# Performance work log

Measured on AMD Instinct MI355X. Metric: run time of the kernel, lower is better.

Reference implementation:

```python
import jax, jax.numpy as jnp
import numpy as np

# Geometry constants (from config)
H, D_BOT, P, K, D = 4096, 1024, 8, 64, 64
SCALE = 1.0


def setup_inputs() -> dict:
    key = jax.random.key(0)
    ks = jax.random.split(key, 20)
    B, T = 4, 2048

    def lin(k, din, dout, s=0.02):
        kw, kb = jax.random.split(k)
        return (jax.random.normal(kw, (din, dout), jnp.float32) * s,
                jax.random.normal(kb, (dout,), jnp.float32) * s)

    x = jax.random.normal(ks[0], (B, T, H), jnp.float32)
    Wi, bi = lin(ks[1], H, D_BOT)
    Wb, bb = lin(ks[2], D_BOT, P * D)          # base_coord_proj
    Wf, bf = lin(ks[3], D_BOT, P * K)          # fiber_section_proj
    Wl, bl = lin(ks[4], D_BOT, P * (D + K))    # lambda_term_proj
    Ww, bw = lin(ks[5], D_BOT, P)              # mixture_proj_w
    Wm, bm = lin(ks[6], D_BOT, P * D)          # mixture_proj_m
    Ws, bs = lin(ks[7], D_BOT, P * D)          # mixture_proj_s
    Wu, bu = lin(ks[8], D_BOT, P * K)          # mixture_proj_u
    Wo, bo = lin(ks[9], D + K, H)              # output_proj
    return dict(x=x, Wi=Wi, bi=bi, Wb=Wb, bb=bb, Wf=Wf, bf=bf, Wl=Wl, bl=bl,
                Ww=Ww, bw=bw, Wm=Wm, bm=bm, Ws=Ws, bs=bs, Wu=Wu, bu=bu,
                Wo=Wo, bo=bo)


def reference(x, Wi, bi, Wb, bb, Wf, bf, Wl, bl, Ww, bw, Wm, bm, Ws, bs, Wu, bu, Wo, bo):
    B, T, _ = x.shape
    # Shared bottleneck
    h_bot = jnp.einsum('bth,hd->btd', x, Wi) + bi                      # (B,T,D_bot)

    # Fan-out of small parallel projections (fused-QKV-like opportunity)
    base_coords = (jnp.einsum('btd,de->bte', h_bot, Wb) + bb).reshape(B, T, P, D)
    base_coords = jnp.clip(base_coords, -10.0, 10.0)
    fiber_sections = (jnp.einsum('btd,de->bte', h_bot, Wf) + bf).reshape(B, T, P, K)
    lambda_terms = (jnp.einsum('btd,de->bte', h_bot, Wl) + bl).reshape(B, T, P, D + K)
    w_logits = jnp.einsum('btd,dp->btp', h_bot, Ww) + bw               # (B,T,P)
    m = (jnp.einsum('btd,de->bte', h_bot, Wm) + bm).reshape(B, T, P, D)
    log_s = jnp.clip((jnp.einsum('btd,de->bte', h_bot, Ws) + bs).reshape(B, T, P, D), -5.0, 5.0)
    u = (jnp.einsum('btd,de->bte', h_bot, Wu) + bu).reshape(B, T, P, K)

    # Lambda operations / info-geometric update treated as identity (undefined in source)
    updated_sections = fiber_sections

    # Parallel transport correction along the T axis: curr - 0.1*(curr - prev)
    prev = base_coords[:, :-1]
    curr = base_coords[:, 1:]
    transported = jnp.concatenate(
        [base_coords[:, :1], curr - 0.1 * (curr - prev)], axis=1)       # (B,T,P,D)
    updated_coords = transported

    # Mixture aggregation
    weights = jax.nn.softmax(w_logits, axis=-1)                         # (B,T,P)
    agg_coords = jnp.einsum('btp,btpd->btd', weights, updated_coords)   # (B,T,D)
    agg_sections = jnp.einsum('btp,btpk->btk', weights, updated_sections)  # (B,T,K)

    combined = jnp.concatenate([agg_coords, agg_sections], axis=-1)     # (B,T,D+K)
    output = jnp.einsum('bte,eh->bth', combined, Wo) + bo               # (B,T,H)
    return x + SCALE * output
```

## Files before the change

### kernel.cpp

```cpp
#include <hip/hip_runtime.h>
#include <hip/hip_bf16.h>
#include <stdint.h>

typedef __hip_bfloat16 bf16;
typedef __attribute__((ext_vector_type(8))) short short8;
typedef __attribute__((ext_vector_type(4))) short short4_t;
typedef __attribute__((ext_vector_type(4))) float float4_t;

__device__ __forceinline__ short f2b_bits(float f) {
  union { float f; unsigned u; } v; v.f = f;
  unsigned r = (v.u + 0x7FFF + ((v.u >> 16) & 1)) >> 16;
  return (short)r;
}
__device__ __forceinline__ bf16 f2b(float f) {
  short s = f2b_bits(f);
  bf16 h; __builtin_memcpy(&h, &s, 2);
  return h;
}
__device__ __forceinline__ bf16 ld_bf16(const void* p, size_t idx, int f32) {
  if (f32) return f2b(((const float*)p)[idx]);
  return ((const bf16*)p)[idx];
}

__device__ __forceinline__ void gload_lds16(const void* g, void* l) {
  __builtin_amdgcn_global_load_lds(
      (const __attribute__((address_space(1))) void*)g,
      (__attribute__((address_space(3))) void*)l, 16, 0, 0);
}

__global__ void detect_dtype(const void* probe, int* flag) {
  int lane = threadIdx.x;
  const unsigned short* u = (const unsigned short*)probe;
  const float* fp = (const float*)probe;
  int cb = 0, cf = 0;
  for (int j = lane; j < 256; j += 64) {
    unsigned short he = u[2 * j];
    int e = (he >> 7) & 0xFF;
    cb += (e >= 0x60 && e <= 0x7E);
    float af = fabsf(fp[j]);
    cf += (af > 1e-9f && af < 1.0f);
  }
#pragma unroll
  for (int off = 32; off > 0; off >>= 1) {
    cb += __shfl_down(cb, off);
    cf += __shfl_down(cf, off);
  }
  if (lane == 0) *flag = (cf > cb) ? 1 : 0;
}

__global__ __launch_bounds__(256) void cvt_x(const void* __restrict__ x,
                                             bf16* __restrict__ xb,
                                             const int* __restrict__ flagp,
                                             size_t n) {
  const int f32 = *flagp;
  size_t i = ((size_t)blockIdx.x * 256 + threadIdx.x) * 8;
  size_t stride = (size_t)gridDim.x * 256 * 8;
  for (; i < n; i += stride) {
    if (f32) {
      const float* xp = (const float*)x + i;
      float4_t f0 = *(const float4_t*)xp;
      float4_t f1 = *(const float4_t*)(xp + 4);
      short8 v;
      v[0] = f2b_bits(f0[0]); v[1] = f2b_bits(f0[1]);
      v[2] = f2b_bits(f0[2]); v[3] = f2b_bits(f0[3]);
      v[4] = f2b_bits(f1[0]); v[5] = f2b_bits(f1[1]);
      v[6] = f2b_bits(f1[2]); v[7] = f2b_bits(f1[3]);
      *(short8*)(xb + i) = v;
    } else {
      *(short8*)(xb + i) = *(const short8*)((const bf16*)x + i);
    }
  }
}

__global__ __launch_bounds__(256) void transpose_all(
    const void* __restrict__ Wi, const void* __restrict__ Wb,
    const void* __restrict__ Wf, const void* __restrict__ Wo,
    bf16* __restrict__ WiT, bf16* __restrict__ WbfT2, bf16* __restrict__ WoT,
    const int* __restrict__ flagp)
{
  const int f32 = *flagp;
  int b = blockIdx.x;
  const void* src; bf16* dst; int K, N, tb;
  if (b < 1024)      { src = Wi; dst = WiT;              K = 4096; N = 1024; tb = b; }
  else if (b < 1152) { src = Wb; dst = WbfT2;            K = 1024; N = 512;  tb = b - 1024; }
  else if (b < 1280) { src = Wf; dst = WbfT2 + 512*1024; K = 1024; N = 512;  tb = b - 1152; }
  else               { src = Wo; dst = WoT;              K = 128;  N = 4096; tb = b - 1280; }
  int nbk = K >> 6;
  int kb = (tb % nbk) * 64, nb = (tb / nbk) * 64;
  __shared__ bf16 tile[64][65];
  int tx = threadIdx.x & 63;
  int ty = threadIdx.x >> 6;
#pragma unroll
  for (int i = 0; i < 64; i += 4)
    tile[ty + i][tx] = ld_bf16(src, (size_t)(kb + ty + i) * N + nb + tx, f32);
  __syncthreads();
#pragma unroll
  for (int i = 0; i < 64; i += 4)
    dst[(size_t)(nb + ty + i) * K + kb + tx] = tile[tx][ty + i];
}

__global__ __launch_bounds__(256) void cvt_small(
    const void* __restrict__ Ww, const void* __restrict__ bw,
    const void* __restrict__ bi, const void* __restrict__ bb,
    const void* __restrict__ bf_, const void* __restrict__ bo,
    bf16* __restrict__ WbfT2, bf16* __restrict__ bbf2,
    bf16* __restrict__ biC, bf16* __restrict__ boC,
    const int* __restrict__ flagp)
{
  const int f32 = *flagp;
  int i = blockIdx.x * 256 + threadIdx.x;
  if (i < 131072) {
    int r = i >> 10, k = i & 1023;
    bf16 v = (r < 8) ? ld_bf16(Ww, (size_t)k * 8 + r, f32) : f2b(0.f);
    WbfT2[(size_t)(1024 + r) * 1024 + k] = v;
  }
  if (i < 128) bbf2[1024 + i] = (i < 8) ? ld_bf16(bw, i, f32) : f2b(0.f);
  if (i < 1024) biC[i] = ld_bf16(bi, i, f32);
  if (i < 512)  bbf2[i] = ld_bf16(bb, i, f32);
  if (i < 512)  bbf2[512 + i] = ld_bf16(bf_, i, f32);
  if (i < 4096) boC[i] = ld_bf16(bo, i, f32);
}

__device__ __forceinline__ void epilogue_64x128(
    char* smem, float4_t (&acc)[2][4], const bf16* bias, const void* resid,
    void* C, int rf32, int cf32, int m0, int n0, int N, int clip_cols,
    int tid, int lane, int wm, int wn, int lm)
{
  float* EP = (float*)smem;
  const int ep_c = (tid & 15) * 4;
#pragma unroll
  for (int h = 0; h < 2; h++) {
    if ((wn >> 6) == h) {
#pragma unroll
      for (int mi = 0; mi < 2; mi++)
#pragma unroll
        for (int ni = 0; ni < 4; ni++) {
          int cl = (wn - h * 64) + ni * 16 + lm;
#pragma unroll
          for (int r = 0; r < 4; r++) {
            int rw = wm + mi * 16 + (lane >> 4) * 4 + r;
            EP[rw * 68 + cl] = acc[mi][ni][r];
          }
        }
    }
    __syncthreads();
#pragma unroll
    for (int i = 0; i < 4; i++) {
      int rw  = (tid >> 4) + 16 * i;
      int gr  = m0 + rw;
      int col = n0 + h * 64 + ep_c;
      size_t idx = (size_t)gr * N + col;
      float4_t v = *(const float4_t*)(EP + rw * 68 + ep_c);
      float o[4];
#pragma unroll
      for (int j = 0; j < 4; j++) {
        float t = v[j] + __bfloat162float(bias[col + j]);
        if (col + j < clip_cols) t = fminf(fmaxf(t, -10.f), 10.f);
        o[j] = t;
      }
      if (resid) {
        if (rf32) {
          float4_t rv = *(const float4_t*)((const float*)resid + idx);
#pragma unroll
          for (int j = 0; j < 4; j++) o[j] += rv[j];
        } else {
          short4_t rv = *(const short4_t*)((const bf16*)resid + idx);
#pragma unroll
          for (int j = 0; j < 4; j++) {
            bf16 hb; short sb = rv[j]; __builtin_memcpy(&hb, &sb, 2);
            o[j] += __bfloat162float(hb);
          }
        }
      }
      if (cf32) {
        *(float4_t*)((float*)C + idx) = (float4_t){o[0], o[1], o[2], o[3]};
      } else {
        short4_t pv;
#pragma unroll
        for (int j = 0; j < 4; j++) pv[j] = f2b_bits(o[j]);
        *(short4_t*)((bf16*)C + idx) = pv;
      }
    }
    __syncthreads();
  }
}

__device__ __forceinline__ void gemm_core_db(
    const bf16* __restrict__ A,
    const bf16* __restrict__ BT,
    const bf16* __restrict__ bias,
    const void* __restrict__ resid,
    void* __restrict__ C,
    const int* __restrict__ rF32, const int* __restrict__ cF32,
    int M, int N, int K, int clip_cols)
{
  constexpr int BM = 64, BN = 128;
  __shared__ alignas(16) char smem[2 * (BM + BN) * 64 * 2];
  bf16* As0 = (bf16*)smem;
  bf16* As1 = (bf16*)(smem + 16384 / 2);
  bf16* Bs0 = (bf16*)(smem + 16384);
  bf16* Bs1 = (bf16*)(smem + 16384 + 16384);
  const int rf32 = rF32 ? *rF32 : 0;
  const int cf32 = cF32 ? *cF32 : 0;
  const int tid  = threadIdx.x;
  const int wave = tid >> 6;
  const int lane = tid & 63;
  const int m0 = blockIdx.x * BM;
  const int n0 = blockIdx.y * BN;
  const int wm = (wave >> 1) * (BM / 2);
  const int wn = (wave & 1) * (BN / 2);
  const int lm = lane & 15;
  const int lk = (lane >> 4) * 8;

  auto stage = [&](bf16* as, bf16* bs, int k0) {
#pragma unroll
    for (int i = 0; i < BN / 32; i++) {
      int V = tid + 256 * i;
      gload_lds16(BT + (size_t)(n0 + (V >> 3)) * K + k0 + (V & 7) * 8,
                  bs + (size_t)V * 8);
    }
#pragma unroll
    for (int i = 0; i < BM / 32; i++) {
      int V = tid + 256 * i;
      gload_lds16(A + (size_t)(m0 + (V >> 3)) * K + k0 + (V & 7) * 8,
                  as + (size_t)V * 8);
    }
  };

  float4_t acc[2][4];
#pragma unroll
  for (int i = 0; i < 2; i++)
#pragma unroll
    for (int j = 0; j < 4; j++) acc[i][j] = (float4_t){0.f, 0.f, 0.f, 0.f};

  const int NT = K >> 6;
  stage(As0, Bs0, 0);

  for (int t = 0; t < NT; t++) {
    bf16* Asc = (t & 1) ? As1 : As0;
    bf16* Bsc = (t & 1) ? Bs1 : Bs0;
    if (t + 1 < NT) {
      stage((t & 1) ? As0 : As1, (t & 1) ? Bs0 : Bs1, (t + 1) << 6);
      asm volatile("s_waitcnt vmcnt(6)" ::: "memory");
    } else {
      asm volatile("s_waitcnt vmcnt(0)" ::: "memory");
    }
    __builtin_amdgcn_sched_barrier(0);
    __builtin_amdgcn_s_barrier();
    __builtin_amdgcn_sched_barrier(0);
#pragma unroll
    for (int kk = 0; kk < 64; kk += 32) {
      short8 af[2], bfr[4];
#pragma unroll
      for (int mi = 0; mi < 2; mi++)
        af[mi] = *(const short8*)(Asc + (wm + mi * 16 + lm) * 64 + kk + lk);
#pragma unroll
      for (int ni = 0; ni < 4; ni++)
        bfr[ni] = *(const short8*)(Bsc + (wn + ni * 16 + lm) * 64 + kk + lk);
#pragma unroll
      for (int mi = 0; mi < 2; mi++)
#pragma unroll
        for (int ni = 0; ni < 4; ni++)
          acc[mi][ni] = __builtin_amdgcn_mfma_f32_16x16x32_bf16(
              af[mi], bfr[ni], acc[mi][ni], 0, 0, 0);
    }
    __builtin_amdgcn_sched_barrier(0);
    __builtin_amdgcn_s_barrier();
  }
  epilogue_64x128(smem, acc, bias, resid, C, rf32, cf32,
                  m0, n0, N, clip_cols, tid, lane, wm, wn, lm);
}

__device__ __forceinline__ void gemm_core_sb(
    const void* __restrict__ A, const bf16* __restrict__ BT,
    const bf16* __restrict__ bias, const void* __restrict__ resid,
    void* __restrict__ C, const int* __restrict__ aF32,
    const int* __restrict__ rF32, const int* __restrict__ cF32,
    int M, int N, int K, int clip_cols)
{
  constexpr int BM = 64, BN = 128;
  __shared__ alignas(16) char smem[(BM + BN) * 64 * 2];
  bf16* As = (bf16*)smem;
  bf16* Bs = (bf16*)smem + BM * 64;
  const int af32 = aF32 ? *aF32 : 0;
  const int rf32 = rF32 ? *rF32 : 0;
  const int cf32 = cF32 ? *cF32 : 0;
  const int tid  = threadIdx.x;
  const int wave = tid >> 6;
  const int lane = tid & 63;
  const int m0 = blockIdx.x * BM;
  const int n0 = blockIdx.y * BN;
  const int wm = (wave >> 1) * (BM / 2);
  const int wn = (wave & 1) * (BN / 2);
  const int lm = lane & 15;
  const int lk = (lane >> 4) * 8;

  float4_t acc[2][4];
#pragma unroll
  for (int i = 0; i < 2; i++)
#pragma unroll
    for (int j = 0; j < 4; j++) acc[i][j] = (float4_t){0.f, 0.f, 0.f, 0.f};

  for (int k0 = 0; k0 < K; k0 += 64) {
#pragma unroll
    for (int i = 0; i < BN / 32; i++) {
      int V = tid + 256 * i;
      gload_lds16(BT + (size_t)(n0 + (V >> 3)) * K + k0 + (V & 7) * 8,
                  Bs + (size_t)V * 8);
    }
#pragma unroll
    for (int i = 0; i < BM / 32; i++) {
      int V = tid + 256 * i;
      int row = V >> 3, kc = (V & 7) * 8;
      if (af32) {
        const float* ap = (const float*)A + (size_t)(m0 + row) * K + k0 + kc;
        float4_t f0 = *(const float4_t*)ap;
        float4_t f1 = *(const float4_t*)(ap + 4);
        short8 v;
        v[0] = f2b_bits(f0[0]); v[1] = f2b_bits(f0[1]);
        v[2] = f2b_bits(f0[2]); v[3] = f2b_bits(f0[3]);
        v[4] = f2b_bits(f1[0]); v[5] = f2b_bits(f1[1]);
        v[6] = f2b_bits(f1[2]); v[7] = f2b_bits(f1[3]);
        *(short8*)(As + (size_t)V * 8) = v;
      } else {
        gload_lds16((const bf16*)A + (size_t)(m0 + row) * K + k0 + kc,
                    As + (size_t)V * 8);
      }
    }
    __syncthreads();
#pragma unroll
    for (int kk = 0; kk < 64; kk += 32) {
      short8 af[2], bfr[4];
#pragma unroll
      for (int mi = 0; mi < 2; mi++)
        af[mi] = *(const short8*)(As + (wm + mi * 16 + lm) * 64 + kk + lk);
#pragma unroll
      for (int ni = 0; ni < 4; ni++)
        bfr[ni] = *(const short8*)(Bs + (wn + ni * 16 + lm) * 64 + kk + lk);
#pragma unroll
      for (int mi = 0; mi < 2; mi++)
#pragma unroll
        for (int ni = 0; ni < 4; ni++)
          acc[mi][ni] = __builtin_amdgcn_mfma_f32_16x16x32_bf16(
              af[mi], bfr[ni], acc[mi][ni], 0, 0, 0);
    }
    __syncthreads();
  }
  epilogue_64x128(smem, acc, bias, resid, C, rf32, cf32,
                  m0, n0, N, clip_cols, tid, lane, wm, wn, lm);
}

__global__ __launch_bounds__(256) void gemm_x(
    const bf16* A, const bf16* BT, const bf16* bias, const void* resid,
    void* C, const int* rF32, const int* cF32, int M, int N, int K, int clip_cols) {
  gemm_core_db(A, BT, bias, resid, C, rF32, cF32, M, N, K, clip_cols);
}
__global__ __launch_bounds__(256) void gemm_x_f(
    const void* A, const bf16* BT, const bf16* bias, const void* resid,
    void* C, const int* aF32, const int* rF32, const int* cF32,
    int M, int N, int K, int clip_cols) {
  gemm_core_sb(A, BT, bias, resid, C, aF32, rF32, cF32, M, N, K, clip_cols);
}
__global__ __launch_bounds__(256) void gemm_h(
    const bf16* A, const bf16* BT, const bf16* bias, const void* resid,
    void* C, const int* rF32, const int* cF32, int M, int N, int K, int clip_cols) {
  gemm_core_db(A, BT, bias, resid, C, rF32, cF32, M, N, K, clip_cols);
}
__global__ __launch_bounds__(256) void gemm_o(
    const bf16* A, const bf16* BT, const bf16* bias, const void* resid,
    void* C, const int* rF32, const int* cF32, int M, int N, int K, int clip_cols) {
  gemm_core_db(A, BT, bias, resid, C, rF32, cF32, M, N, K, clip_cols);
}

__global__ __launch_bounds__(128) void build_combined(
    const bf16* __restrict__ bcfs,
    bf16* __restrict__ comb)
{
  int t = blockIdx.x;
  int tid = threadIdx.x;
  int tl = t & 2047;
  __shared__ float lg[8];
  __shared__ float w[8];
  if (tid < 8) lg[tid] = __bfloat162float(bcfs[(size_t)t * 1152 + 1024 + tid]);
  __syncthreads();
  if (tid < 8) {
    float mx = lg[0];
#pragma unroll
    for (int i = 1; i < 8; i++) mx = fmaxf(mx, lg[i]);
    float den = 0.f;
#pragma unroll
    for (int i = 0; i < 8; i++) den += expf(lg[i] - mx);
    w[tid] = expf(lg[tid] - mx) / den;
  }
  __syncthreads();
  float s = 0.f;
  if (tid < 64) {
    int d = tid;
    const bf16* bc = bcfs + (size_t)t * 1152;
    size_t tp = (tl == 0) ? (size_t)t : (size_t)t - 1;
    const bf16* bp = bcfs + tp * 1152;
#pragma unroll
    for (int p = 0; p < 8; p++) {
      float cur = __bfloat162float(bc[p * 64 + d]);
      float v = (tl == 0) ? cur : (0.9f * cur + 0.1f * __bfloat162float(bp[p * 64 + d]));
      s += w[p] * v;
    }
  } else {
    int d = tid - 64;
    const bf16* fsrow = bcfs + (size_t)t * 1152 + 512;
#pragma unroll
    for (int p = 0; p < 8; p++) s += w[p] * __bfloat162float(fsrow[p * 64 + d]);
  }
  comb[(size_t)t * 128 + tid] = __float2bfloat16(s);
}

extern "C" void kernel_launch(void* const* d_in, const int* in_sizes, int n_in,
                              void* d_out, int out_size, void* d_ws, size_t ws_size,
                              hipStream_t stream) {
  (void)in_sizes; (void)n_in; (void)out_size;
  const void* x   = d_in[0];
  const void* Wi  = d_in[1];
  const void* bi  = d_in[2];
  const void* Wb  = d_in[3];
  const void* bb  = d_in[4];
  const void* Wf  = d_in[5];
  const void* bfv = d_in[6];
  const void* Ww  = d_in[9];
  const void* bw  = d_in[10];
  const void* Wo  = d_in[17];
  const void* bo  = d_in[18];

  char* ws = (char*)d_ws;
  bf16*  h_bot = (bf16*)(ws + 0);
  bf16*  comb  = (bf16*)(ws + 0);
  bf16*  bcfs  = (bf16*)(ws + 16777216);
  bf16*  WiT   = (bf16*)(ws + 35651584);
  bf16*  WbfT2 = (bf16*)(ws + 44040192);
  bf16*  WoT   = (bf16*)(ws + 46399488);
  bf16*  biC   = (bf16*)(ws + 47448064);
  bf16*  bbf2C = (bf16*)(ws + 47450112);
  bf16*  boC   = (bf16*)(ws + 47452416);
  int*   flag  = (int*)(ws + 47460608);
  bf16*  xb    = (bf16*)(ws + 47464448);
  const bool use_xb = ws_size >= (size_t)47464448 + 67108864;

  detect_dtype<<<1, 64, 0, stream>>>(bi, flag);

  if (use_xb)
    cvt_x<<<2048, 256, 0, stream>>>(x, xb, flag, (size_t)8192 * 4096);

  transpose_all<<<1408, 256, 0, stream>>>(Wi, Wb, Wf, Wo, WiT, WbfT2, WoT, flag);
  cvt_small<<<512, 256, 0, stream>>>(Ww, bw, bi, bb, bfv, bo,
                                     WbfT2, bbf2C, biC, boC, flag);

  if (use_xb)
    gemm_x<<<dim3(128, 8), 256, 0, stream>>>(
        xb, WiT, biC, nullptr, h_bot, nullptr, nullptr,
        8192, 1024, 4096, 0);
  else
    gemm_x_f<<<dim3(128, 8), 256, 0, stream>>>(
        x, WiT, biC, nullptr, h_bot, flag, nullptr, nullptr,
        8192, 1024, 4096, 0);
  gemm_h<<<dim3(128, 9), 256, 0, stream>>>(
      h_bot, WbfT2, bbf2C, nullptr, bcfs, nullptr, nullptr,
      8192, 1152, 1024, 512);
  build_combined<<<8192, 128, 0, stream>>>(bcfs, comb);
  gemm_o<<<dim3(128, 32), 256, 0, stream>>>(
      comb, WoT, boC, x, d_out, flag, flag,
      8192, 4096, 128, 0);
}
```

Before: 528.2 us.

## Stage A tile through registers and fuse x conversion into transpose kernel

```diff
diff --git a/kernel.cpp b/kernel.cpp
--- a/kernel.cpp
+++ b/kernel.cpp
@@ -48,38 +48,36 @@
   if (lane == 0) *flag = (cf > cb) ? 1 : 0;
 }
 
-__global__ __launch_bounds__(256) void cvt_x(const void* __restrict__ x,
-                                             bf16* __restrict__ xb,
-                                             const int* __restrict__ flagp,
-                                             size_t n) {
-  const int f32 = *flagp;
-  size_t i = ((size_t)blockIdx.x * 256 + threadIdx.x) * 8;
-  size_t stride = (size_t)gridDim.x * 256 * 8;
-  for (; i < n; i += stride) {
-    if (f32) {
-      const float* xp = (const float*)x + i;
-      float4_t f0 = *(const float4_t*)xp;
-      float4_t f1 = *(const float4_t*)(xp + 4);
-      short8 v;
-      v[0] = f2b_bits(f0[0]); v[1] = f2b_bits(f0[1]);
-      v[2] = f2b_bits(f0[2]); v[3] = f2b_bits(f0[3]);
-      v[4] = f2b_bits(f1[0]); v[5] = f2b_bits(f1[1]);
-      v[6] = f2b_bits(f1[2]); v[7] = f2b_bits(f1[3]);
-      *(short8*)(xb + i) = v;
-    } else {
-      *(short8*)(xb + i) = *(const short8*)((const bf16*)x + i);
-    }
-  }
-}
-
 __global__ __launch_bounds__(256) void transpose_all(
     const void* __restrict__ Wi, const void* __restrict__ Wb,
     const void* __restrict__ Wf, const void* __restrict__ Wo,
     bf16* __restrict__ WiT, bf16* __restrict__ WbfT2, bf16* __restrict__ WoT,
+    const void* __restrict__ x, bf16* __restrict__ xb,
     const int* __restrict__ flagp)
 {
   const int f32 = *flagp;
   int b = blockIdx.x;
+  if (b >= 1408) {
+    size_t base = (size_t)(b - 1408) * 16384;
+#pragma unroll
+    for (int j = 0; j < 8; j++) {
+      size_t i = base + (size_t)j * 2048 + threadIdx.x * 8;
+      if (f32) {
+        const float* xp = (const float*)x + i;
+        float4_t f0 = *(const float4_t*)xp;
+        float4_t f1 = *(const float4_t*)(xp + 4);
+        short8 v;
+        v[0] = f2b_bits(f0[0]); v[1] = f2b_bits(f0[1]);
+        v[2] = f2b_bits(f0[2]); v[3] = f2b_bits(f0[3]);
+        v[4] = f2b_bits(f1[0]); v[5] = f2b_bits(f1[1]);
+        v[6] = f2b_bits(f1[2]); v[7] = f2b_bits(f1[3]);
+        *(short8*)(xb + i) = v;
+      } else {
+        *(short8*)(xb + i) = *(const short8*)((const bf16*)x + i);
+      }
+    }
+    return;
+  }
   const void* src; bf16* dst; int K, N, tb;
   if (b < 1024)      { src = Wi; dst = WiT;              K = 4096; N = 1024; tb = b; }
   else if (b < 1152) { src = Wb; dst = WbfT2;            K = 1024; N = 512;  tb = b - 1024; }
@@ -185,21 +183,17 @@
   }
 }
 
-__device__ __forceinline__ void gemm_core_db(
-    const bf16* __restrict__ A,
-    const bf16* __restrict__ BT,
-    const bf16* __restrict__ bias,
-    const void* __restrict__ resid,
-    void* __restrict__ C,
-    const int* __restrict__ rF32, const int* __restrict__ cF32,
-    int M, int N, int K, int clip_cols)
+__device__ __forceinline__ void gemm_core_db2(
+    const bf16* __restrict__ A, const bf16* __restrict__ BT,
+    const bf16* __restrict__ bias, const void* __restrict__ resid,
+    void* __restrict__ C, const int* __restrict__ rF32,
+    const int* __restrict__ cF32, int M, int N, int K, int clip_cols)
 {
   constexpr int BM = 64, BN = 128;
-  __shared__ alignas(16) char smem[2 * (BM + BN) * 64 * 2];
-  bf16* As0 = (bf16*)smem;
-  bf16* As1 = (bf16*)(smem + 16384 / 2);
-  bf16* Bs0 = (bf16*)(smem + 16384);
-  bf16* Bs1 = (bf16*)(smem + 16384 + 16384);
+  __shared__ alignas(16) char smem[(BM * 64 + 2 * BN * 64) * 2];
+  bf16* As  = (bf16*)smem;
+  bf16* Bs0 = (bf16*)(smem + BM * 64 * 2);
+  bf16* Bs1 = (bf16*)(smem + BM * 64 * 2 + BN * 64 * 2);
   const int rf32 = rF32 ? *rF32 : 0;
   const int cf32 = cF32 ? *cF32 : 0;
   const int tid  = threadIdx.x;
@@ -212,19 +206,28 @@
   const int lm = lane & 15;
   const int lk = (lane >> 4) * 8;
 
-  auto stage = [&](bf16* as, bf16* bs, int k0) {
-#pragma unroll
-    for (int i = 0; i < BN / 32; i++) {
+  short8 areg[2];
+  auto loadA = [&](int k0) {
+#pragma unroll
+    for (int i = 0; i < 2; i++) {
+      int V = tid + 256 * i;
+      areg[i] = *(const short8*)(A + (size_t)(m0 + (V >> 3)) * K + k0 + (V & 7) * 8);
+    }
+  };
+  auto writeA = [&]() {
+#pragma unroll
+    for (int i = 0; i < 2; i++) {
+      int V = tid + 256 * i;
+      *(short8*)(As + (size_t)V * 8) = areg[i];
+    }
+  };
+  auto issueB = [&](bf16* bs, int k0) {
+#pragma unroll
+    for (int i = 0; i < 4; i++) {
       int V = tid + 256 * i;
       gload_lds16(BT + (size_t)(n0 + (V >> 3)) * K + k0 + (V & 7) * 8,
                   bs + (size_t)V * 8);
     }
-#pragma unroll
-    for (int i = 0; i < BM / 32; i++) {
-      int V = tid + 256 * i;
-      gload_lds16(A + (size_t)(m0 + (V >> 3)) * K + k0 + (V & 7) * 8,
-                  as + (size_t)V * 8);
-    }
   };
 
   float4_t acc[2][4];
@@ -234,26 +237,33 @@
     for (int j = 0; j < 4; j++) acc[i][j] = (float4_t){0.f, 0.f, 0.f, 0.f};
 
   const int NT = K >> 6;
-  stage(As0, Bs0, 0);
+  loadA(0);
+  issueB(Bs0, 0);
+  asm volatile("s_waitcnt vmcnt(4)" ::: "memory");
+  __builtin_amdgcn_sched_barrier(0);
+  writeA();
+  asm volatile("s_waitcnt lgkmcnt(0)" ::: "memory");
+  __builtin_amdgcn_sched_barrier(0);
+  __builtin_amdgcn_s_barrier();
+  __builtin_amdgcn_sched_barrier(0);
 
   for (int t = 0; t < NT; t++) {
-    bf16* Asc = (t & 1) ? As1 : As0;
     bf16* Bsc = (t & 1) ? Bs1 : Bs0;
-    if (t + 1 < NT) {
-      stage((t & 1) ? As0 : As1, (t & 1) ? Bs0 : Bs1, (t + 1) << 6);
+    const bool pf = (t + 1 < NT);
+    if (pf) {
+      loadA((t + 1) << 6);
+      issueB((t & 1) ? Bs0 : Bs1, (t + 1) << 6);
       asm volatile("s_waitcnt vmcnt(6)" ::: "memory");
     } else {
       asm volatile("s_waitcnt vmcnt(0)" ::: "memory");
     }
     __builtin_amdgcn_sched_barrier(0);
-    __builtin_amdgcn_s_barrier();
-    __builtin_amdgcn_sched_barrier(0);
 #pragma unroll
     for (int kk = 0; kk < 64; kk += 32) {
       short8 af[2], bfr[4];
 #pragma unroll
       for (int mi = 0; mi < 2; mi++)
-        af[mi] = *(const short8*)(Asc + (wm + mi * 16 + lm) * 64 + kk + lk);
+        af[mi] = *(const short8*)(As + (wm + mi * 16 + lm) * 64 + kk + lk);
 #pragma unroll
       for (int ni = 0; ni < 4; ni++)
         bfr[ni] = *(const short8*)(Bsc + (wn + ni * 16 + lm) * 64 + kk + lk);
@@ -266,6 +276,16 @@
     }
     __builtin_amdgcn_sched_barrier(0);
     __builtin_amdgcn_s_barrier();
+    __builtin_amdgcn_sched_barrier(0);
+    if (pf) {
+      asm volatile("s_waitcnt vmcnt(4)" ::: "memory");
+      __builtin_amdgcn_sched_barrier(0);
+      writeA();
+      asm volatile("s_waitcnt lgkmcnt(0)" ::: "memory");
+      __builtin_amdgcn_sched_barrier(0);
+    }
+    __builtin_amdgcn_s_barrier();
+    __builtin_amdgcn_sched_barrier(0);
   }
   epilogue_64x128(smem, acc, bias, resid, C, rf32, cf32,
                   m0, n0, N, clip_cols, tid, lane, wm, wn, lm);
@@ -303,13 +323,13 @@
 
   for (int k0 = 0; k0 < K; k0 += 64) {
 #pragma unroll
-    for (int i = 0; i < BN / 32; i++) {
+    for (int i = 0; i < 4; i++) {
       int V = tid + 256 * i;
       gload_lds16(BT + (size_t)(n0 + (V >> 3)) * K + k0 + (V & 7) * 8,
                   Bs + (size_t)V * 8);
     }
 #pragma unroll
-    for (int i = 0; i < BM / 32; i++) {
+    for (int i = 0; i < 2; i++) {
       int V = tid + 256 * i;
       int row = V >> 3, kc = (V & 7) * 8;
       if (af32) {
@@ -353,7 +373,7 @@
 __global__ __launch_bounds__(256) void gemm_x(
     const bf16* A, const bf16* BT, const bf16* bias, const void* resid,
     void* C, const int* rF32, const int* cF32, int M, int N, int K, int clip_cols) {
-  gemm_core_db(A, BT, bias, resid, C, rF32, cF32, M, N, K, clip_cols);
+  gemm_core_db2(A, BT, bias, resid, C, rF32, cF32, M, N, K, clip_cols);
 }
 __global__ __launch_bounds__(256) void gemm_x_f(
     const void* A, const bf16* BT, const bf16* bias, const void* resid,
@@ -364,12 +384,12 @@
 __global__ __launch_bounds__(256) void gemm_h(
     const bf16* A, const bf16* BT, const bf16* bias, const void* resid,
     void* C, const int* rF32, const int* cF32, int M, int N, int K, int clip_cols) {
-  gemm_core_db(A, BT, bias, resid, C, rF32, cF32, M, N, K, clip_cols);
+  gemm_core_db2(A, BT, bias, resid, C, rF32, cF32, M, N, K, clip_cols);
 }
 __global__ __launch_bounds__(256) void gemm_o(
     const bf16* A, const bf16* BT, const bf16* bias, const void* resid,
     void* C, const int* rF32, const int* cF32, int M, int N, int K, int clip_cols) {
-  gemm_core_db(A, BT, bias, resid, C, rF32, cF32, M, N, K, clip_cols);
+  gemm_core_sb(A, BT, bias, resid, C, nullptr, rF32, cF32, M, N, K, clip_cols);
 }
 
 __global__ __launch_bounds__(128) void build_combined(
@@ -446,10 +466,8 @@
 
   detect_dtype<<<1, 64, 0, stream>>>(bi, flag);
 
-  if (use_xb)
-    cvt_x<<<2048, 256, 0, stream>>>(x, xb, flag, (size_t)8192 * 4096);
-
-  transpose_all<<<1408, 256, 0, stream>>>(Wi, Wb, Wf, Wo, WiT, WbfT2, WoT, flag);
+  transpose_all<<<use_xb ? 3456 : 1408, 256, 0, stream>>>(
+      Wi, Wb, Wf, Wo, WiT, WbfT2, WoT, x, xb, flag);
   cvt_small<<<512, 256, 0, stream>>>(Ww, bw, bi, bb, bfv, bo,
                                      WbfT2, bbf2C, biC, boC, flag);
 
```

Result: no change. 528.3 us (+0.0%).
